# Kernel optimization log

Measured on AMD Instinct MI355X. Metric: run time of the kernel, lower is better.

Reference implementation:

```python
import jax, jax.numpy as jnp
import numpy as np

HEAD, D_MODEL, D_KV, D_FF = 12, 768, 64, 3072
BS, S = 8, 512
D_K = D_MODEL // HEAD


def layer_norm(x, g, b, eps=1e-5):
    m = jnp.mean(x, axis=-1, keepdims=True)
    v = jnp.var(x, axis=-1, keepdims=True)
    return (x - m) / jnp.sqrt(v + eps) * g + b


def setup_inputs() -> dict:
    key = jax.random.key(0)
    ks = jax.random.split(key, 16)
    w = lambda k, *s: (jax.random.normal(k, s, dtype=jnp.float32) * 0.02)
    return {
        'x': jax.random.normal(ks[0], (BS, S, D_MODEL), dtype=jnp.float32),
        'pad_mask': jnp.ones((BS, S), dtype=bool),
        'prior': jnp.zeros((1, 1, 1, 1), dtype=jnp.float32),
        # GroupAttention params
        'ga_ln_g': jnp.ones((D_MODEL,), jnp.float32), 'ga_ln_b': jnp.zeros((D_MODEL,), jnp.float32),
        'ga_wq': w(ks[1], D_K, D_K), 'ga_bq': jnp.zeros((D_K,), jnp.float32),
        'ga_wk': w(ks[2], D_K, D_K), 'ga_bk': jnp.zeros((D_K,), jnp.float32),
        # ScaledDotProductAttention params (head*d_kv == d_model)
        'sa_wq': w(ks[3], HEAD * D_KV, D_MODEL), 'sa_bq': jnp.zeros((HEAD * D_KV,), jnp.float32),
        'sa_wk': w(ks[4], HEAD * D_KV, D_MODEL), 'sa_bk': jnp.zeros((HEAD * D_KV,), jnp.float32),
        'sa_wv': w(ks[5], HEAD * D_KV, D_MODEL), 'sa_bv': jnp.zeros((HEAD * D_KV,), jnp.float32),
        # FFN params
        'ff_w1': w(ks[6], D_FF, D_MODEL), 'ff_b1': jnp.zeros((D_FF,), jnp.float32),
        'ff_w2': w(ks[7], D_MODEL, D_FF), 'ff_b2': jnp.zeros((D_MODEL,), jnp.float32),
        # Sublayer (pre-)norms
        'sl0_g': jnp.ones((D_MODEL,), jnp.float32), 'sl0_b': jnp.zeros((D_MODEL,), jnp.float32),
        'sl1_g': jnp.ones((D_MODEL,), jnp.float32), 'sl1_b': jnp.zeros((D_MODEL,), jnp.float32),
    }


def group_attention(x, pad_mask, prior, ln_g, ln_b, wq, bq, wk, bk):
    bs, s = x.shape[:2]
    ctx = layer_norm(x, ln_g, ln_b).reshape(bs, s, HEAD, D_K).transpose(0, 2, 1, 3)  # [bs,h,s,dk]
    a = jnp.eye(s, k=1, dtype=jnp.float32)   # superdiag
    c = jnp.eye(s, k=-1, dtype=jnp.float32)  # subdiag
    diag = jnp.eye(s, dtype=bool)
    tridiag = (a + c) > 0
    mask = pad_mask[:, None, None, :] & tridiag[None, None]  # [bs,1,s,s]
    q = ctx @ wq.T + bq
    k = ctx @ wk.T + bk
    scores = jnp.einsum('bhqd,bhkd->bhqk', q, k) / D_K
    scores = jnp.where(mask, scores, -10000.0)
    na = jax.nn.softmax(scores, axis=-1)
    na = jnp.sqrt(na * na.swapaxes(-2, -1) + 1e-4)
    na = prior + (1.0 - prior) * na
    tri = jnp.triu(jnp.ones((s, s), jnp.float32))  # upper incl diag
    # keep log-values only on the superdiagonal, zero elsewhere
    t = jnp.where(a[None, None] > 0, jnp.log(na + 1e-9), 0.0) @ tri
    g = jnp.exp(tri @ t)
    # zero where tri - eye == 0 (diagonal and strict lower) -> keep strict upper
    g = jnp.where((tri - jnp.eye(s, dtype=jnp.float32))[None, None] == 0, 0.0, g)
    g_attn = g + g.swapaxes(-2, -1) + jnp.where(diag[None, None], na, 1e-4)
    return g_attn, na


def self_attention(xn, group_prob, wq, bq, wk, bk, wv, bv):
    bs, s = xn.shape[:2]
    q = (xn @ wq.T + bq).reshape(bs, s, HEAD, D_KV).transpose(0, 2, 1, 3)
    k = (xn @ wk.T + bk).reshape(bs, s, HEAD, D_KV).transpose(0, 2, 1, 3)
    v = (xn @ wv.T + bv).reshape(bs, s, HEAD, D_KV).transpose(0, 2, 1, 3)
    att = jnp.einsum('bhqd,bhkd->bhqk', q, k) / np.sqrt(D_KV).astype(np.float32)
    # NOTE: original uses non-inplace att.masked_fill(...) without assignment -> mask has no effect
    att = jax.nn.softmax(att, axis=-1) * group_prob
    out = jnp.einsum('bhqk,bhkd->bhqd', att, v)
    return out.transpose(0, 2, 1, 3).reshape(bs, s, HEAD * D_KV)


def reference(x, pad_mask, prior,
              ga_ln_g, ga_ln_b, ga_wq, ga_bq, ga_wk, ga_bk,
              sa_wq, sa_bq, sa_wk, sa_bk, sa_wv, sa_bv,
              ff_w1, ff_b1, ff_w2, ff_b2,
              sl0_g, sl0_b, sl1_g, sl1_b):
    group_prob, break_prob = group_attention(x, pad_mask, prior,
                                             ga_ln_g, ga_ln_b, ga_wq, ga_bq, ga_wk, ga_bk)
    # sublayer 0: pre-norm residual around self-attn weighted by group_prob
    x = x + self_attention(layer_norm(x, sl0_g, sl0_b), group_prob,
                           sa_wq, sa_bq, sa_wk, sa_bk, sa_wv, sa_bv)
    # sublayer 1: pre-norm residual around FFN
    h = jax.nn.relu(layer_norm(x, sl1_g, sl1_b) @ ff_w1.T + ff_b1)
    x = x + (h @ ff_w2.T + ff_b2)
    return (x, group_prob, break_prob)
```

## Files before the change

### kernel.cpp

```cpp
#include <hip/hip_runtime.h>
#include <hip/hip_bf16.h>

#define HEADS 12
#define DM    768
#define DKH   64
#define DFF   3072
#define BSZ   8
#define SEQ   512
#define MROWS (BSZ*SEQ)
#define BH    (BSZ*HEADS)

typedef __attribute__((ext_vector_type(8))) short bf16x8;
typedef __attribute__((ext_vector_type(4))) float f32x4;

__device__ __forceinline__ void gload_lds16(const ushort* g, ushort* l) {
  __builtin_amdgcn_global_load_lds(
      (const __attribute__((address_space(1))) unsigned int*)g,
      (__attribute__((address_space(3))) unsigned int*)l, 16, 0, 0);
}

__device__ __forceinline__ float b2f(ushort u) {
  union { unsigned int i; float f; } c; c.i = (unsigned int)u << 16; return c.f;
}

__global__ __launch_bounds__(256) void ln_cvt_kernel(
    const float* __restrict__ x,
    const float* __restrict__ g0, const float* __restrict__ b0, __hip_bfloat16* __restrict__ ln0,
    const float* __restrict__ gg, const float* __restrict__ gb, __hip_bfloat16* __restrict__ lnga,
    const float* __restrict__ swq, const float* __restrict__ swk, const float* __restrict__ swv,
    const float* __restrict__ w1s, const float* __restrict__ w2s,
    __hip_bfloat16* __restrict__ dqkv, __hip_bfloat16* __restrict__ d1,
    __hip_bfloat16* __restrict__ d2) {
  int t = threadIdx.x;
  if (blockIdx.x >= 1024) {
    long gid = (long)(blockIdx.x - 1024)*256 + t;
    long i = gid*4;
    const float* s; __hip_bfloat16* d; long off;
    if (i < 1769472L) {
      long j = i / 589824L; off = i - j*589824L;
      s = (j == 0) ? swq : (j == 1) ? swk : swv;
      d = dqkv + j*589824L;
    } else if (i < 4128768L) {
      off = i - 1769472L; s = w1s; d = d1;
    } else {
      off = i - 4128768L; s = w2s; d = d2;
    }
    float4 v = *(const float4*)(s + off);
    d[off+0] = __float2bfloat16(v.x);
    d[off+1] = __float2bfloat16(v.y);
    d[off+2] = __float2bfloat16(v.z);
    d[off+3] = __float2bfloat16(v.w);
    return;
  }
  int lane = t & 63, w = t >> 6;
  int row = blockIdx.x*4 + w;
  size_t base = (size_t)row * DM;
  float v[12]; float s = 0.f, s2 = 0.f;
  #pragma unroll
  for (int i = 0; i < 12; ++i) {
    v[i] = x[base + lane + 64*i];
    s += v[i]; s2 += v[i]*v[i];
  }
  #pragma unroll
  for (int off = 1; off < 64; off <<= 1) {
    s  += __shfl_xor(s,  off, 64);
    s2 += __shfl_xor(s2, off, 64);
  }
  float mean = s * (1.f/DM);
  float rstd = rsqrtf(s2 * (1.f/DM) - mean*mean + 1e-5f);
  #pragma unroll
  for (int i = 0; i < 12; ++i) {
    int c = lane + 64*i;
    float h = (v[i]-mean)*rstd;
    ln0[base + c]  = __float2bfloat16(h*g0[c] + b0[c]);
    lnga[base + c] = __float2bfloat16(h*gg[c] + gb[c]);
  }
}

__global__ __launch_bounds__(256) void ga_proj_mfma_kernel(
    const __hip_bfloat16* __restrict__ lnga,
    const float* __restrict__ wq, const float* __restrict__ bq,
    const float* __restrict__ wk, const float* __restrict__ bk,
    float* __restrict__ Qg, float* __restrict__ Kg) {
  __shared__ ushort WQ[64*72];
  __shared__ ushort WK[64*72];
  int t = threadIdx.x;
  int h  = blockIdx.x >> 4;
  int r0 = (blockIdx.x & 15) * 256;
  for (int i = t; i < 4096; i += 256) {
    int d = i >> 6, c = i & 63;
    __hip_bfloat16 q = __float2bfloat16(wq[i]);
    __hip_bfloat16 k = __float2bfloat16(wk[i]);
    WQ[d*72 + c] = *(ushort*)&q;
    WK[d*72 + c] = *(ushort*)&k;
  }
  __syncthreads();
  int lane = t & 63, w = t >> 6;
  int lrow = lane & 15, lhi = lane >> 4;
  const ushort* Ag = (const ushort*)lnga;
  bf16x8 a[4][2];
  #pragma unroll
  for (int i = 0; i < 4; ++i)
    #pragma unroll
    for (int ks = 0; ks < 2; ++ks)
      a[i][ks] = *(const bf16x8*)(Ag + (size_t)(r0 + w*64 + i*16 + lrow)*DM + h*64 + ks*32 + lhi*8);
  int b = r0 >> 9;
  {
    bf16x8 bf[4][2];
    #pragma unroll
    for (int j = 0; j < 4; ++j)
      #pragma unroll
      for (int ks = 0; ks < 2; ++ks)
        bf[j][ks] = *(const bf16x8*)&WQ[(j*16 + lrow)*72 + ks*32 + lhi*8];
    f32x4 acc[4][4] = {};
    #pragma unroll
    for (int i = 0; i < 4; ++i)
      #pragma unroll
      for (int j = 0; j < 4; ++j) {
        acc[i][j] = __builtin_amdgcn_mfma_f32_16x16x32_bf16(a[i][0], bf[j][0], acc[i][j], 0, 0, 0);
        acc[i][j] = __builtin_amdgcn_mfma_f32_16x16x32_bf16(a[i][1], bf[j][1], acc[i][j], 0, 0, 0);
      }
    #pragma unroll
    for (int i = 0; i < 4; ++i) {
      int rowb = r0 + w*64 + i*16 + lhi*4;
      #pragma unroll
      for (int j = 0; j < 4; ++j) {
        int d = j*16 + lrow;
        float bias = bq[d];
        #pragma unroll
        for (int r = 0; r < 4; ++r) {
          int sIdx = (rowb + r) & 511;
          Qg[(((size_t)b*HEADS + h)*SEQ + sIdx)*DKH + d] = acc[i][j][r] + bias;
        }
      }
    }
  }
  {
    bf16x8 bf[4][2];
    #pragma unroll
    for (int j = 0; j < 4; ++j)
      #pragma unroll
      for (int ks = 0; ks < 2; ++ks)
        bf[j][ks] = *(const bf16x8*)&WK[(j*16 + lrow)*72 + ks*32 + lhi*8];
    f32x4 acc[4][4] = {};
    #pragma unroll
    for (int i = 0; i < 4; ++i)
      #pragma unroll
      for (int j = 0; j < 4; ++j) {
        acc[i][j] = __builtin_amdgcn_mfma_f32_16x16x32_bf16(a[i][0], bf[j][0], acc[i][j], 0, 0, 0);
        acc[i][j] = __builtin_amdgcn_mfma_f32_16x16x32_bf16(a[i][1], bf[j][1], acc[i][j], 0, 0, 0);
      }
    #pragma unroll
    for (int i = 0; i < 4; ++i) {
      int rowb = r0 + w*64 + i*16 + lhi*4;
      #pragma unroll
      for (int j = 0; j < 4; ++j) {
        int d = j*16 + lrow;
        float bias = bk[d];
        #pragma unroll
        for (int r = 0; r < 4; ++r) {
          int sIdx = (rowb + r) & 511;
          Kg[(((size_t)b*HEADS + h)*SEQ + sIdx)*DKH + d] = acc[i][j][r] + bias;
        }
      }
    }
  }
}

__global__ __launch_bounds__(512) void ga_edges_kernel(
    const float* __restrict__ Qg, const float* __restrict__ Kg,
    const float* __restrict__ prior, float* __restrict__ nsWS, float* __restrict__ cumWS) {
  __shared__ float pu[SEQ], pd[SEQ];
  __shared__ float wsum[8], wpre[8];
  int bh = blockIdx.x, m = threadIdx.x;
  const float* Qb = Qg + (size_t)bh*SEQ*DKH;
  const float* Kb = Kg + (size_t)bh*SEQ*DKH;
  const float4* qm = (const float4*)(Qb + (size_t)m*DKH);
  float su = -1e4f, sd = -1e4f;
  if (m < SEQ-1) {
    const float4* kn = (const float4*)(Kb + (size_t)(m+1)*DKH);
    float a = 0.f;
    #pragma unroll
    for (int i = 0; i < 16; ++i) {
      float4 q4 = qm[i], k4 = kn[i];
      a += q4.x*k4.x + q4.y*k4.y + q4.z*k4.z + q4.w*k4.w;
    }
    su = a * (1.f/DKH);
  }
  if (m >= 1) {
    const float4* kp = (const float4*)(Kb + (size_t)(m-1)*DKH);
    float a = 0.f;
    #pragma unroll
    for (int i = 0; i < 16; ++i) {
      float4 q4 = qm[i], k4 = kp[i];
      a += q4.x*k4.x + q4.y*k4.y + q4.z*k4.z + q4.w*k4.w;
    }
    sd = a * (1.f/DKH);
  }
  float mx = fmaxf(su, sd);
  float eu = __expf(su - mx), ed = __expf(sd - mx);
  float inv = 1.f / (eu + ed);
  pu[m] = eu * inv;
  pd[m] = ed * inv;
  __syncthreads();
  float pr = prior[0];
  float nsv = 0.f, lg = 0.f;
  if (m < SEQ-1) {
    float vv = sqrtf(pu[m]*pd[m+1] + 1e-4f);
    nsv = pr + (1.f - pr)*vv;
    lg = __logf(nsv + 1e-9f);
  }
  float v = lg;
  #pragma unroll
  for (int off = 1; off < 64; off <<= 1) {
    float u = __shfl_up(v, off, 64);
    if ((m & 63) >= off) v += u;
  }
  if ((m & 63) == 63) wsum[m >> 6] = v;
  __syncthreads();
  if (m == 0) {
    float a = 0.f;
    #pragma unroll
    for (int i = 0; i < 8; ++i) { wpre[i] = a; a += wsum[i]; }
  }
  __syncthreads();
  float incl = v + wpre[m >> 6];
  nsWS[(size_t)bh*SEQ + m] = nsv;
  cumWS[(size_t)bh*SEQ + m] = incl - lg;
}

template<int MODE>
__global__ __launch_bounds__(512, 2) void gemm256_kernel(
    const __hip_bfloat16* __restrict__ A, const __hip_bfloat16* __restrict__ B,
    const float* __restrict__ b0, const float* __restrict__ b1, const float* __restrict__ b2,
    __hip_bfloat16* __restrict__ C,
    const float* __restrict__ nsWS, const float* __restrict__ cumWS,
    const float* __restrict__ prior, float* __restrict__ gp, float* __restrict__ bp,
    int gbBase) {
  constexpr int N    = (MODE==0) ? 2304 : (MODE==1) ? 3072 : 768;
  constexpr int TN   = N / 256;
  constexpr int LDAB = (MODE==2) ? 3072 : 768;
  constexpr int NT   = (MODE==0) ? 144 : (MODE==1) ? 192 : 48;
  __shared__ ushort LDS[65536];
  int t = threadIdx.x;
  int bidx = blockIdx.x;
  if (MODE != 2 && bidx >= NT) {
    int gbBlk = gbBase + (bidx - NT);
    int bh = gbBlk >> 7;
    int q  = ((gbBlk & 127) << 2) | (t >> 7);
    int tt = t & 127;
    const float* cum = cumWS + (size_t)bh*SEQ;
    const float* ns  = nsWS  + (size_t)bh*SEQ;
    float pr = prior[0];
    float c0 = pr + (1.f - pr)*0.01f;
    float cq = cum[q];
    size_t rb = ((size_t)bh*SEQ + q)*SEQ;
    int k0 = tt*4;
    float4 g4, b4;
    float* gv = (float*)&g4; float* bv = (float*)&b4;
    #pragma unroll
    for (int j = 0; j < 4; ++j) {
      int k = k0 + j;
      float g;
      if (k == q) g = c0;
      else {
        float c = cum[k];
        g = __expf((k > q) ? (c - cq) : (cq - c)) + 1e-4f;
      }
      float bb = c0;
      if (k == q+1)      bb = ns[q];
      else if (k+1 == q) bb = ns[q-1];
      gv[j] = g; bv[j] = bb;
    }
    *(float4*)(gp + rb + k0) = g4;
    *(float4*)(bp + rb + k0) = b4;
    return;
  }
  int lane = t & 63, w = t >> 6;
  int rin = lane >> 3, gr = lane & 7;
  int lrow = lane & 15, lhi = lane >> 4;
  int tile = (bidx & 7)*(NT/8) + (bidx >> 3);
  int m0 = (tile / TN) * 256;
  int n0 = (tile % TN) * 256;
  int kOff = (MODE == 2) ? blockIdx.y * 768 : 0;
  if (MODE == 2) C += (size_t)blockIdx.y * MROWS * 768;
  int wr = w >> 2, wc = w & 3;
  const ushort* Ag = (const ushort*)A;
  const ushort* Bg = (const ushort*)B;
  f32x4 acc[8][4] = {};
  auto STAGE = [&](int p, int kt) {
    int k0 = kOff + kt*64;
    ushort* Ad = &LDS[p*16384];
    ushort* Bd = &LDS[32768 + p*16384];
    int cs = (gr ^ rin) * 8;
    #pragma unroll
    for (int q = 0; q < 4; ++q) {
      int rr = q*64 + w*8 + rin;
      gload_lds16(Ag + (size_t)(m0 + rr)*LDAB + k0 + cs, &Ad[(q*64 + w*8)*64]);
      gload_lds16(Bg + (size_t)(n0 + rr)*LDAB + k0 + cs, &Bd[(q*64 + w*8)*64]);
    }
  };
  const int nt = 12;
  STAGE(0, 0);
  STAGE(1, 1);
  asm volatile("s_waitcnt vmcnt(8)" ::: "memory");
  __builtin_amdgcn_s_barrier();
  int p = 0;
  for (int kt = 0; kt < nt; ++kt) {
    const ushort* Ar = &LDS[p*16384];
    const ushort* Br = &LDS[32768 + p*16384];
    int sw0 = (lhi ^ (lrow & 7)) * 8;
    int sw1 = ((4 + lhi) ^ (lrow & 7)) * 8;
    bf16x8 a0[8], b0r[4], a1[8], b1r[4];
    #pragma unroll
    for (int i = 0; i < 8; ++i)
      a0[i] = *(const bf16x8*)&Ar[(wr*128 + i*16 + lrow)*64 + sw0];
    #pragma unroll
    for (int j = 0; j < 4; ++j)
      b0r[j] = *(const bf16x8*)&Br[(wc*64 + j*16 + lrow)*64 + sw0];
    #pragma unroll
    for (int i = 0; i < 8; ++i)
      #pragma unroll
      for (int j = 0; j < 4; ++j)
        acc[i][j] = __builtin_amdgcn_mfma_f32_16x16x32_bf16(a0[i], b0r[j], acc[i][j], 0, 0, 0);
    #pragma unroll
    for (int i = 0; i < 8; ++i)
      a1[i] = *(const bf16x8*)&Ar[(wr*128 + i*16 + lrow)*64 + sw1];
    #pragma unroll
    for (int j = 0; j < 4; ++j)
      b1r[j] = *(const bf16x8*)&Br[(wc*64 + j*16 + lrow)*64 + sw1];
    asm volatile("s_waitcnt lgkmcnt(0)" ::: "memory");
    __builtin_amdgcn_sched_barrier(0);
    __builtin_amdgcn_s_barrier();
    if (kt + 2 < nt) STAGE(p, kt + 2);
    __builtin_amdgcn_s_setprio(1);
    #pragma unroll
    for (int i = 0; i < 8; ++i)
      #pragma unroll
      for (int j = 0; j < 4; ++j)
        acc[i][j] = __builtin_amdgcn_mfma_f32_16x16x32_bf16(a1[i], b1r[j], acc[i][j], 0, 0, 0);
    __builtin_amdgcn_s_setprio(0);
    if (kt + 1 < nt) {
      if (kt + 2 < nt) asm volatile("s_waitcnt vmcnt(8)" ::: "memory");
      else             asm volatile("s_waitcnt vmcnt(0)" ::: "memory");
      __builtin_amdgcn_s_barrier();
    }
    p ^= 1;
  }
  #pragma unroll
  for (int i = 0; i < 8; ++i) {
    int grow = m0 + wr*128 + i*16 + lhi*4;
    #pragma unroll
    for (int j = 0; j < 4; ++j) {
      int gcol = n0 + wc*64 + j*16 + lrow;
      float bvv;
      if (MODE == 0)      bvv = (gcol < 768) ? b0[gcol] : (gcol < 1536) ? b1[gcol-768] : b2[gcol-1536];
      else if (MODE == 1) bvv = b0[gcol];
      else                bvv = 0.f;
      #pragma unroll
      for (int r = 0; r < 4; ++r) {
        float v = acc[i][j][r] + bvv;
        if (MODE == 1) v = fmaxf(v, 0.f);
        C[(size_t)(grow + r)*N + gcol] = __float2bfloat16(v);
      }
    }
  }
}

__global__ __launch_bounds__(256) void vt_kernel(
    const __hip_bfloat16* __restrict__ qkv, __hip_bfloat16* __restrict__ vT) {
  int gid = blockIdx.x*256 + threadIdx.x;
  int o = gid*8;
  int bh = o >> 15;
  int rem = o & 32767;
  int d = rem >> 9;
  int s0 = rem & 511;
  int b = bh / HEADS, h = bh % HEADS;
  const ushort* src = (const ushort*)qkv + ((size_t)(b*SEQ + s0))*2304 + 1536 + h*64 + d;
  ushort tmp[8];
  #pragma unroll
  for (int j = 0; j < 8; ++j) tmp[j] = src[(size_t)j*2304];
  *(bf16x8*)((ushort*)vT + (size_t)bh*32768 + d*512 + s0) = *(bf16x8*)tmp;
}

__global__ __launch_bounds__(256) void ffn2_reduce_kernel(
    const __hip_bfloat16* __restrict__ p, const float* __restrict__ bias,
    float* __restrict__ out) {
  int gid = blockIdx.x*256 + threadIdx.x;
  size_t i = (size_t)gid*8;
  const ushort* pp = (const ushort*)p;
  float acc[8];
  int col = (int)(i % DM);
  #pragma unroll
  for (int j = 0; j < 8; ++j) acc[j] = bias[col + j];
  #pragma unroll
  for (int s = 0; s < 4; ++s) {
    bf16x8 v = *(const bf16x8*)(pp + (size_t)s*MROWS*DM + i);
    #pragma unroll
    for (int j = 0; j < 8; ++j) acc[j] += b2f((ushort)v[j]);
  }
  float4 o0 = *(const float4*)(out + i);
  float4 o1 = *(const float4*)(out + i + 4);
  o0.x += acc[0]; o0.y += acc[1]; o0.z += acc[2]; o0.w += acc[3];
  o1.x += acc[4]; o1.y += acc[5]; o1.z += acc[6]; o1.w += acc[7];
  *(float4*)(out + i)     = o0;
  *(float4*)(out + i + 4) = o1;
}

__global__ __launch_bounds__(256) void ln_res_kernel(
    const float* __restrict__ x, const __hip_bfloat16* __restrict__ a, float* __restrict__ xs,
    const float* __restrict__ g, const float* __restrict__ b, __hip_bfloat16* __restrict__ o) {
  __shared__ float lds[16];
  int row = blockIdx.x, t = threadIdx.x;
  size_t base = (size_t)row * DM;
  float v0 = x[base+t]     + __bfloat162float(a[base+t]);
  float v1 = x[base+t+256] + __bfloat162float(a[base+t+256]);
  float v2 = x[base+t+512] + __bfloat162float(a[base+t+512]);
  xs[base+t] = v0; xs[base+t+256] = v1; xs[base+t+512] = v2;
  float s = v0 + v1 + v2, s2 = v0*v0 + v1*v1 + v2*v2;
  #pragma unroll
  for (int off = 32; off > 0; off >>= 1) {
    s  += __shfl_down(s,  off, 64);
    s2 += __shfl_down(s2, off, 64);
  }
  int w = t >> 6, ln = t & 63;
  if (ln == 0) { lds[w*2] = s; lds[w*2+1] = s2; }
  __syncthreads();
  if (t == 0) {
    float aa = 0.f, bb = 0.f;
    for (int i = 0; i < 4; ++i) { aa += lds[i*2]; bb += lds[i*2+1]; }
    lds[0] = aa; lds[1] = bb;
  }
  __syncthreads();
  s = lds[0]; s2 = lds[1];
  float mean = s * (1.f/DM);
  float rstd = rsqrtf(s2 * (1.f/DM) - mean*mean + 1e-5f);
  o[base+t]     = __float2bfloat16((v0-mean)*rstd*g[t]     + b[t]);
  o[base+t+256] = __float2bfloat16((v1-mean)*rstd*g[t+256] + b[t+256]);
  o[base+t+512] = __float2bfloat16((v2-mean)*rstd*g[t+512] + b[t+512]);
}

__global__ __launch_bounds__(256) void attn_mfma_kernel(
    const __hip_bfloat16* __restrict__ qk, const __hip_bfloat16* __restrict__ vT,
    const float* __restrict__ cumWS, const float* __restrict__ prior,
    __hip_bfloat16* __restrict__ att) {
  __shared__ ushort Ps[4][16][72];
  int t = threadIdx.x;
  int lane = t & 63, wid = t >> 6;
  int bid = blockIdx.x + blockIdx.y * 8;
  int tile = (bid & 7)*96 + (bid >> 3);
  int qt = tile & 7, bh = tile >> 3;
  int b = bh / HEADS, h = bh % HEADS;
  int lrow = lane & 15, lhi = lane >> 4;
  int qbase = qt*64 + wid*16;
  const ushort* qg = (const ushort*)qk;
  bf16x8 aq[2];
  {
    const ushort* qp = qg + (size_t)(b*SEQ + qbase + lrow)*2304 + h*64 + lhi*8;
    aq[0] = *(const bf16x8*)qp;
    aq[1] = *(const bf16x8*)(qp + 32);
  }
  const float* cum = cumWS + (size_t)bh*SEQ;
  float pr = prior[0];
  float c0 = pr + (1.f - pr)*0.01f;
  int qrow[4]; float cq[4];
  #pragma unroll
  for (int r = 0; r < 4; ++r) { qrow[r] = qbase + lhi*4 + r; cq[r] = cum[qrow[r]]; }
  float lsum[4] = {0.f, 0.f, 0.f, 0.f};
  f32x4 oacc[4] = {};
  const ushort* kg = qg + 768;
  const ushort* vg = (const ushort*)vT;
  for (int kt = 0; kt < 8; ++kt) {
    f32x4 sacc[4] = {};
    #pragma unroll
    for (int j = 0; j < 4; ++j) {
      const ushort* kp = kg + (size_t)(b*SEQ + kt*64 + j*16 + lrow)*2304 + h*64 + lhi*8;
      bf16x8 bk0 = *(const bf16x8*)kp;
      bf16x8 bk1 = *(const bf16x8*)(kp + 32);
      sacc[j] = __builtin_amdgcn_mfma_f32_16x16x32_bf16(aq[0], bk0, sacc[j], 0, 0, 0);
      sacc[j] = __builtin_amdgcn_mfma_f32_16x16x32_bf16(aq[1], bk1, sacc[j], 0, 0, 0);
    }
    float ck[4];
    #pragma unroll
    for (int j = 0; j < 4; ++j) ck[j] = cum[kt*64 + j*16 + lrow];
    #pragma unroll
    for (int j = 0; j < 4; ++j) {
      int kk = kt*64 + j*16 + lrow;
      #pragma unroll
      for (int r = 0; r < 4; ++r) {
        float e = __expf(fminf(sacc[j][r]*0.125f - 16.f, 60.f));
        lsum[r] += e;
        float dd = ck[j] - cq[r];
        float gpv = (kk == qrow[r]) ? c0 : (__expf((kk > qrow[r]) ? dd : -dd) + 1e-4f);
        __hip_bfloat16 pb = __float2bfloat16(e * gpv);
        Ps[wid][lhi*4 + r][j*16 + lrow] = *(ushort*)&pb;
      }
    }
    asm volatile("s_waitcnt lgkmcnt(0)" ::: "memory");
    #pragma unroll
    for (int c = 0; c < 2; ++c) {
      bf16x8 ap = *(const bf16x8*)&Ps[wid][lrow][c*32 + lhi*8];
      #pragma unroll
      for (int dj = 0; dj < 4; ++dj) {
        const ushort* vp = vg + ((size_t)bh*64 + dj*16 + lrow)*512 + kt*64 + c*32 + lhi*8;
        bf16x8 bv = *(const bf16x8*)vp;
        oacc[dj] = __builtin_amdgcn_mfma_f32_16x16x32_bf16(ap, bv, oacc[dj], 0, 0, 0);
      }
    }
  }
  #pragma unroll
  for (int off = 1; off < 16; off <<= 1) {
    #pragma unroll
    for (int r = 0; r < 4; ++r) lsum[r] += __shfl_xor(lsum[r], off, 64);
  }
  float inv[4];
  #pragma unroll
  for (int r = 0; r < 4; ++r) inv[r] = 1.f / lsum[r];
  #pragma unroll
  for (int dj = 0; dj < 4; ++dj) {
    #pragma unroll
    for (int r = 0; r < 4; ++r) {
      float v = oacc[dj][r] * inv[r];
      att[(size_t)(b*SEQ + qbase + lhi*4 + r)*DM + h*64 + dj*16 + lrow] = __float2bfloat16(v);
    }
  }
}

extern "C" void kernel_launch(void* const* d_in, const int* in_sizes, int n_in,
                              void* d_out, int out_size, void* d_ws, size_t ws_size,
                              hipStream_t stream) {
  const float* x      = (const float*)d_in[0];
  const float* prior  = (const float*)d_in[2];
  const float* ga_g   = (const float*)d_in[3];
  const float* ga_b   = (const float*)d_in[4];
  const float* ga_wq  = (const float*)d_in[5];
  const float* ga_bq  = (const float*)d_in[6];
  const float* ga_wk  = (const float*)d_in[7];
  const float* ga_bk  = (const float*)d_in[8];
  const float* sa_wq  = (const float*)d_in[9];
  const float* sa_bq  = (const float*)d_in[10];
  const float* sa_wk  = (const float*)d_in[11];
  const float* sa_bk  = (const float*)d_in[12];
  const float* sa_wv  = (const float*)d_in[13];
  const float* sa_bv  = (const float*)d_in[14];
  const float* ff_w1  = (const float*)d_in[15];
  const float* ff_b1  = (const float*)d_in[16];
  const float* ff_w2  = (const float*)d_in[17];
  const float* ff_b2  = (const float*)d_in[18];
  const float* sl0_g  = (const float*)d_in[19];
  const float* sl0_b  = (const float*)d_in[20];
  const float* sl1_g  = (const float*)d_in[21];
  const float* sl1_b  = (const float*)d_in[22];

  float* out_x  = (float*)d_out;
  float* out_gp = out_x  + (size_t)MROWS*DM;
  float* out_bp = out_gp + (size_t)BH*SEQ*SEQ;

  char* W = (char*)d_ws;
  __hip_bfloat16* ln0    = (__hip_bfloat16*)(W + 0);
  __hip_bfloat16* lnga   = (__hip_bfloat16*)(W + 6291456);
  float* Qg   = (float*)(W + 12582912);
  float* Kg   = (float*)(W + 25165824);
  __hip_bfloat16* qkv3   = (__hip_bfloat16*)(W + 37748736);
  __hip_bfloat16* vT     = (__hip_bfloat16*)(W + 56623104);
  __hip_bfloat16* attbuf = (__hip_bfloat16*)(W + 62914560);
  __hip_bfloat16* ln1    = (__hip_bfloat16*)(W + 69206016);
  __hip_bfloat16* wqkv   = (__hip_bfloat16*)(W + 75497472);
  __hip_bfloat16* w1     = (__hip_bfloat16*)(W + 79036416);
  __hip_bfloat16* w2     = (__hip_bfloat16*)(W + 83755008);
  __hip_bfloat16* hbuf   = (__hip_bfloat16*)(W + 88473600);
  __hip_bfloat16* parts  = (__hip_bfloat16*)(W + 113639424);
  float* nsWS  = (float*)(W + 138805248);
  float* cumWS = (float*)(W + 139001856);

  ln_cvt_kernel<<<7360, 256, 0, stream>>>(
      x, sl0_g, sl0_b, ln0, ga_g, ga_b, lnga,
      sa_wq, sa_wk, sa_wv, ff_w1, ff_w2, wqkv, w1, w2);
  ga_proj_mfma_kernel<<<192, 256, 0, stream>>>(lnga, ga_wq, ga_bq, ga_wk, ga_bk, Qg, Kg);
  ga_edges_kernel<<<BH, SEQ, 0, stream>>>(Qg, Kg, prior, nsWS, cumWS);
  gemm256_kernel<0><<<144 + 6144, 512, 0, stream>>>(
      ln0, wqkv, sa_bq, sa_bk, sa_bv, qkv3,
      nsWS, cumWS, prior, out_gp, out_bp, 0);
  vt_kernel<<<3072, 256, 0, stream>>>(qkv3, vT);
  attn_mfma_kernel<<<dim3(8, BH), 256, 0, stream>>>(qkv3, vT, cumWS, prior, attbuf);
  ln_res_kernel<<<MROWS, 256, 0, stream>>>(x, attbuf, out_x, sl1_g, sl1_b, ln1);
  gemm256_kernel<1><<<192 + 6144, 512, 0, stream>>>(
      ln1, w1, ff_b1, nullptr, nullptr, hbuf,
      nsWS, cumWS, prior, out_gp, out_bp, 6144);
  gemm256_kernel<2><<<dim3(48, 4), 512, 0, stream>>>(
      hbuf, w2, nullptr, nullptr, nullptr, parts,
      nullptr, nullptr, nullptr, nullptr, nullptr, 0);
  ffn2_reduce_kernel<<<1536, 256, 0, stream>>>(parts, ff_b2, out_x);
}
```

Measured before the change: 279.1 us.

## Fuse GA projection into QKV GEMM, transpose V in epilogue, spread gp/bp writes

```diff
diff --git a/kernel.cpp b/kernel.cpp
--- a/kernel.cpp
+++ b/kernel.cpp
@@ -21,6 +21,69 @@
 
 __device__ __forceinline__ float b2f(ushort u) {
   union { unsigned int i; float f; } c; c.i = (unsigned int)u << 16; return c.f;
+}
+
+__device__ __forceinline__ void gb_rows_512(
+    int row, int t, const float* __restrict__ nsWS, const float* __restrict__ cumWS,
+    const float* __restrict__ prior, float* __restrict__ gp, float* __restrict__ bp) {
+  int bh = row >> 9, q = row & 511;
+  const float* cum = cumWS + (size_t)bh*SEQ;
+  const float* ns  = nsWS  + (size_t)bh*SEQ;
+  float pr = prior[0];
+  float c0 = pr + (1.f - pr)*0.01f;
+  float cq = cum[q];
+  size_t rb = ((size_t)bh*SEQ + q)*SEQ;
+  int k0 = (t & 127)*4;
+  float4 g4, b4;
+  float* gv = (float*)&g4; float* bv = (float*)&b4;
+  #pragma unroll
+  for (int j = 0; j < 4; ++j) {
+    int k = k0 + j;
+    float g;
+    if (k == q) g = c0;
+    else {
+      float c = cum[k];
+      g = __expf((k > q) ? (c - cq) : (cq - c)) + 1e-4f;
+    }
+    float bb = c0;
+    if (k == q+1)      bb = ns[q];
+    else if (k+1 == q) bb = ns[q-1];
+    gv[j] = g; bv[j] = bb;
+  }
+  *(float4*)(gp + rb + k0) = g4;
+  *(float4*)(bp + rb + k0) = b4;
+}
+
+__device__ __forceinline__ void gb_rows_256(
+    int row, int t, const float* __restrict__ nsWS, const float* __restrict__ cumWS,
+    const float* __restrict__ prior, float* __restrict__ gp, float* __restrict__ bp) {
+  int bh = row >> 9, q = row & 511;
+  const float* cum = cumWS + (size_t)bh*SEQ;
+  const float* ns  = nsWS  + (size_t)bh*SEQ;
+  float pr = prior[0];
+  float c0 = pr + (1.f - pr)*0.01f;
+  float cq = cum[q];
+  size_t rb = ((size_t)bh*SEQ + q)*SEQ;
+  int k0 = (t & 63)*8;
+  float g8[8], b8[8];
+  #pragma unroll
+  for (int j = 0; j < 8; ++j) {
+    int k = k0 + j;
+    float g;
+    if (k == q) g = c0;
+    else {
+      float c = cum[k];
+      g = __expf((k > q) ? (c - cq) : (cq - c)) + 1e-4f;
+    }
+    float bb = c0;
+    if (k == q+1)      bb = ns[q];
+    else if (k+1 == q) bb = ns[q-1];
+    g8[j] = g; b8[j] = bb;
+  }
+  *(float4*)(gp + rb + k0)     = *(float4*)&g8[0];
+  *(float4*)(gp + rb + k0 + 4) = *(float4*)&g8[4];
+  *(float4*)(bp + rb + k0)     = *(float4*)&b8[0];
+  *(float4*)(bp + rb + k0 + 4) = *(float4*)&b8[4];
 }
 
 __global__ __launch_bounds__(256) void ln_cvt_kernel(
@@ -77,96 +140,6 @@
   }
 }
 
-__global__ __launch_bounds__(256) void ga_proj_mfma_kernel(
-    const __hip_bfloat16* __restrict__ lnga,
-    const float* __restrict__ wq, const float* __restrict__ bq,
-    const float* __restrict__ wk, const float* __restrict__ bk,
-    float* __restrict__ Qg, float* __restrict__ Kg) {
-  __shared__ ushort WQ[64*72];
-  __shared__ ushort WK[64*72];
-  int t = threadIdx.x;
-  int h  = blockIdx.x >> 4;
-  int r0 = (blockIdx.x & 15) * 256;
-  for (int i = t; i < 4096; i += 256) {
-    int d = i >> 6, c = i & 63;
-    __hip_bfloat16 q = __float2bfloat16(wq[i]);
-    __hip_bfloat16 k = __float2bfloat16(wk[i]);
-    WQ[d*72 + c] = *(ushort*)&q;
-    WK[d*72 + c] = *(ushort*)&k;
-  }
-  __syncthreads();
-  int lane = t & 63, w = t >> 6;
-  int lrow = lane & 15, lhi = lane >> 4;
-  const ushort* Ag = (const ushort*)lnga;
-  bf16x8 a[4][2];
-  #pragma unroll
-  for (int i = 0; i < 4; ++i)
-    #pragma unroll
-    for (int ks = 0; ks < 2; ++ks)
-      a[i][ks] = *(const bf16x8*)(Ag + (size_t)(r0 + w*64 + i*16 + lrow)*DM + h*64 + ks*32 + lhi*8);
-  int b = r0 >> 9;
-  {
-    bf16x8 bf[4][2];
-    #pragma unroll
-    for (int j = 0; j < 4; ++j)
-      #pragma unroll
-      for (int ks = 0; ks < 2; ++ks)
-        bf[j][ks] = *(const bf16x8*)&WQ[(j*16 + lrow)*72 + ks*32 + lhi*8];
-    f32x4 acc[4][4] = {};
-    #pragma unroll
-    for (int i = 0; i < 4; ++i)
-      #pragma unroll
-      for (int j = 0; j < 4; ++j) {
-        acc[i][j] = __builtin_amdgcn_mfma_f32_16x16x32_bf16(a[i][0], bf[j][0], acc[i][j], 0, 0, 0);
-        acc[i][j] = __builtin_amdgcn_mfma_f32_16x16x32_bf16(a[i][1], bf[j][1], acc[i][j], 0, 0, 0);
-      }
-    #pragma unroll
-    for (int i = 0; i < 4; ++i) {
-      int rowb = r0 + w*64 + i*16 + lhi*4;
-      #pragma unroll
-      for (int j = 0; j < 4; ++j) {
-        int d = j*16 + lrow;
-        float bias = bq[d];
-        #pragma unroll
-        for (int r = 0; r < 4; ++r) {
-          int sIdx = (rowb + r) & 511;
-          Qg[(((size_t)b*HEADS + h)*SEQ + sIdx)*DKH + d] = acc[i][j][r] + bias;
-        }
-      }
-    }
-  }
-  {
-    bf16x8 bf[4][2];
-    #pragma unroll
-    for (int j = 0; j < 4; ++j)
-      #pragma unroll
-      for (int ks = 0; ks < 2; ++ks)
-        bf[j][ks] = *(const bf16x8*)&WK[(j*16 + lrow)*72 + ks*32 + lhi*8];
-    f32x4 acc[4][4] = {};
-    #pragma unroll
-    for (int i = 0; i < 4; ++i)
-      #pragma unroll
-      for (int j = 0; j < 4; ++j) {
-        acc[i][j] = __builtin_amdgcn_mfma_f32_16x16x32_bf16(a[i][0], bf[j][0], acc[i][j], 0, 0, 0);
-        acc[i][j] = __builtin_amdgcn_mfma_f32_16x16x32_bf16(a[i][1], bf[j][1], acc[i][j], 0, 0, 0);
-      }
-    #pragma unroll
-    for (int i = 0; i < 4; ++i) {
-      int rowb = r0 + w*64 + i*16 + lhi*4;
-      #pragma unroll
-      for (int j = 0; j < 4; ++j) {
-        int d = j*16 + lrow;
-        float bias = bk[d];
-        #pragma unroll
-        for (int r = 0; r < 4; ++r) {
-          int sIdx = (rowb + r) & 511;
-          Kg[(((size_t)b*HEADS + h)*SEQ + sIdx)*DKH + d] = acc[i][j][r] + bias;
-        }
-      }
-    }
-  }
-}
-
 __global__ __launch_bounds__(512) void ga_edges_kernel(
     const float* __restrict__ Qg, const float* __restrict__ Kg,
     const float* __restrict__ prior, float* __restrict__ nsWS, float* __restrict__ cumWS) {
@@ -233,57 +206,98 @@
 __global__ __launch_bounds__(512, 2) void gemm256_kernel(
     const __hip_bfloat16* __restrict__ A, const __hip_bfloat16* __restrict__ B,
     const float* __restrict__ b0, const float* __restrict__ b1, const float* __restrict__ b2,
-    __hip_bfloat16* __restrict__ C,
+    __hip_bfloat16* __restrict__ C, __hip_bfloat16* __restrict__ vT,
     const float* __restrict__ nsWS, const float* __restrict__ cumWS,
     const float* __restrict__ prior, float* __restrict__ gp, float* __restrict__ bp,
-    int gbBase) {
+    const __hip_bfloat16* __restrict__ lnga,
+    const float* __restrict__ gwq, const float* __restrict__ gbq,
+    const float* __restrict__ gwk, const float* __restrict__ gbk,
+    float* __restrict__ Qg, float* __restrict__ Kg) {
   constexpr int N    = (MODE==0) ? 2304 : (MODE==1) ? 3072 : 768;
   constexpr int TN   = N / 256;
   constexpr int LDAB = (MODE==2) ? 3072 : 768;
-  constexpr int NT   = (MODE==0) ? 144 : (MODE==1) ? 192 : 48;
+  constexpr int NT   = (MODE==0) ? 144 : (MODE==1) ? 192 : 192;
   __shared__ ushort LDS[65536];
   int t = threadIdx.x;
   int bidx = blockIdx.x;
-  if (MODE != 2 && bidx >= NT) {
-    int gbBlk = gbBase + (bidx - NT);
-    int bh = gbBlk >> 7;
-    int q  = ((gbBlk & 127) << 2) | (t >> 7);
-    int tt = t & 127;
-    const float* cum = cumWS + (size_t)bh*SEQ;
-    const float* ns  = nsWS  + (size_t)bh*SEQ;
-    float pr = prior[0];
-    float c0 = pr + (1.f - pr)*0.01f;
-    float cq = cum[q];
-    size_t rb = ((size_t)bh*SEQ + q)*SEQ;
-    int k0 = tt*4;
-    float4 g4, b4;
-    float* gv = (float*)&g4; float* bv = (float*)&b4;
-    #pragma unroll
-    for (int j = 0; j < 4; ++j) {
-      int k = k0 + j;
-      float g;
-      if (k == q) g = c0;
-      else {
-        float c = cum[k];
-        g = __expf((k > q) ? (c - cq) : (cq - c)) + 1e-4f;
+  if (bidx >= NT) {
+    if (MODE == 0) {
+      ushort* WQ = LDS;
+      ushort* WK = LDS + 4608;
+      for (int i = t; i < 4096; i += 512) {
+        int d = i >> 6, c = i & 63;
+        __hip_bfloat16 q = __float2bfloat16(gwq[i]);
+        __hip_bfloat16 k = __float2bfloat16(gwk[i]);
+        WQ[d*72 + c] = *(ushort*)&q;
+        WK[d*72 + c] = *(ushort*)&k;
       }
-      float bb = c0;
-      if (k == q+1)      bb = ns[q];
-      else if (k+1 == q) bb = ns[q-1];
-      gv[j] = g; bv[j] = bb;
-    }
-    *(float4*)(gp + rb + k0) = g4;
-    *(float4*)(bp + rb + k0) = b4;
+      __syncthreads();
+      int task = (bidx - 144)*2 + (t >> 8);
+      int h  = task >> 4;
+      int r0 = (task & 15) * 256;
+      int t2 = t & 255;
+      int lane = t2 & 63, w = t2 >> 6;
+      int lrow = lane & 15, lhi = lane >> 4;
+      const ushort* Ag2 = (const ushort*)lnga;
+      bf16x8 a[4][2];
+      #pragma unroll
+      for (int i = 0; i < 4; ++i)
+        #pragma unroll
+        for (int ks = 0; ks < 2; ++ks)
+          a[i][ks] = *(const bf16x8*)(Ag2 + (size_t)(r0 + w*64 + i*16 + lrow)*DM + h*64 + ks*32 + lhi*8);
+      int b = r0 >> 9;
+      #pragma unroll
+      for (int qk = 0; qk < 2; ++qk) {
+        const ushort* Wm = qk ? WK : WQ;
+        const float* bias = qk ? gbk : gbq;
+        float* Og = qk ? Kg : Qg;
+        bf16x8 bf[4][2];
+        #pragma unroll
+        for (int j = 0; j < 4; ++j)
+          #pragma unroll
+          for (int ks = 0; ks < 2; ++ks)
+            bf[j][ks] = *(const bf16x8*)&Wm[(j*16 + lrow)*72 + ks*32 + lhi*8];
+        f32x4 acc[4][4] = {};
+        #pragma unroll
+        for (int i = 0; i < 4; ++i)
+          #pragma unroll
+          for (int j = 0; j < 4; ++j) {
+            acc[i][j] = __builtin_amdgcn_mfma_f32_16x16x32_bf16(a[i][0], bf[j][0], acc[i][j], 0, 0, 0);
+            acc[i][j] = __builtin_amdgcn_mfma_f32_16x16x32_bf16(a[i][1], bf[j][1], acc[i][j], 0, 0, 0);
+          }
+        #pragma unroll
+        for (int i = 0; i < 4; ++i) {
+          int rowb = r0 + w*64 + i*16 + lhi*4;
+          #pragma unroll
+          for (int j = 0; j < 4; ++j) {
+            int d = j*16 + lrow;
+            float bv = bias[d];
+            #pragma unroll
+            for (int r = 0; r < 4; ++r) {
+              int sIdx = (rowb + r) & 511;
+              Og[(((size_t)b*HEADS + h)*SEQ + sIdx)*DKH + d] = acc[i][j][r] + bv;
+            }
+          }
+        }
+      }
+    } else {
+      int base = (MODE == 1) ? 16384 : 32768;
+      int row = base + (bidx - NT)*4 + (t >> 7);
+      gb_rows_512(row, t, nsWS, cumWS, prior, gp, bp);
+    }
     return;
   }
   int lane = t & 63, w = t >> 6;
   int rin = lane >> 3, gr = lane & 7;
   int lrow = lane & 15, lhi = lane >> 4;
-  int tile = (bidx & 7)*(NT/8) + (bidx >> 3);
+  int z = 0, tl = bidx;
+  if (MODE == 2) { z = bidx / 48; tl = bidx % 48; }
+  constexpr int NTIL = (MODE==2) ? 48 : NT;
+  int tile = (tl & 7)*(NTIL/8) + (tl >> 3);
   int m0 = (tile / TN) * 256;
   int n0 = (tile % TN) * 256;
-  int kOff = (MODE == 2) ? blockIdx.y * 768 : 0;
-  if (MODE == 2) C += (size_t)blockIdx.y * MROWS * 768;
+  int kOff = (MODE == 2) ? z * 768 : 0;
+  if (MODE == 2) C += (size_t)z * MROWS * 768;
   int wr = w >> 2, wc = w & 3;
   const ushort* Ag = (const ushort*)A;
   const ushort* Bg = (const ushort*)B;
@@ -347,6 +361,40 @@
     }
     p ^= 1;
   }
+  if (MODE == 0 && n0 >= 1536) {
+    ushort* T = LDS;
+    int b = m0 >> 9, s0 = m0 & 511;
+    #pragma unroll
+    for (int ps = 0; ps < 2; ++ps) {
+      if ((wc >> 1) == ps) {
+        #pragma unroll
+        for (int j = 0; j < 4; ++j) {
+          int dl = (wc & 1)*64 + j*16 + lrow;
+          float bvv = b2[n0 - 1536 + ps*128 + dl];
+          #pragma unroll
+          for (int i = 0; i < 8; ++i) {
+            #pragma unroll
+            for (int r = 0; r < 4; ++r) {
+              __hip_bfloat16 hh = __float2bfloat16(acc[i][j][r] + bvv);
+              T[dl*264 + wr*128 + i*16 + lhi*4 + r] = *(ushort*)&hh;
+            }
+          }
+        }
+      }
+      __syncthreads();
+      #pragma unroll
+      for (int it = 0; it < 8; ++it) {
+        int idx = t + 512*it;
+        int dl = idx >> 5, sc8 = (idx & 31)*8;
+        int dg = n0 - 1536 + ps*128 + dl;
+        int h = dg >> 6, dmod = dg & 63;
+        bf16x8 vv = *(const bf16x8*)&T[dl*264 + sc8];
+        *(bf16x8*)((ushort*)vT + ((size_t)(b*HEADS + h)*64 + dmod)*512 + s0 + sc8) = vv;
+      }
+      __syncthreads();
+    }
+    return;
+  }
   #pragma unroll
   for (int i = 0; i < 8; ++i) {
     int grow = m0 + wr*128 + i*16 + lhi*4;
@@ -354,7 +402,7 @@
     for (int j = 0; j < 4; ++j) {
       int gcol = n0 + wc*64 + j*16 + lrow;
       float bvv;
-      if (MODE == 0)      bvv = (gcol < 768) ? b0[gcol] : (gcol < 1536) ? b1[gcol-768] : b2[gcol-1536];
+      if (MODE == 0)      bvv = (gcol < 768) ? b0[gcol] : b1[gcol-768];
       else if (MODE == 1) bvv = b0[gcol];
       else                bvv = 0.f;
       #pragma unroll
@@ -365,22 +413,6 @@
       }
     }
   }
-}
-
-__global__ __launch_bounds__(256) void vt_kernel(
-    const __hip_bfloat16* __restrict__ qkv, __hip_bfloat16* __restrict__ vT) {
-  int gid = blockIdx.x*256 + threadIdx.x;
-  int o = gid*8;
-  int bh = o >> 15;
-  int rem = o & 32767;
-  int d = rem >> 9;
-  int s0 = rem & 511;
-  int b = bh / HEADS, h = bh % HEADS;
-  const ushort* src = (const ushort*)qkv + ((size_t)(b*SEQ + s0))*2304 + 1536 + h*64 + d;
-  ushort tmp[8];
-  #pragma unroll
-  for (int j = 0; j < 8; ++j) tmp[j] = src[(size_t)j*2304];
-  *(bf16x8*)((ushort*)vT + (size_t)bh*32768 + d*512 + s0) = *(bf16x8*)tmp;
 }
 
 __global__ __launch_bounds__(256) void ffn2_reduce_kernel(
@@ -410,45 +442,48 @@
 __global__ __launch_bounds__(256) void ln_res_kernel(
     const float* __restrict__ x, const __hip_bfloat16* __restrict__ a, float* __restrict__ xs,
     const float* __restrict__ g, const float* __restrict__ b, __hip_bfloat16* __restrict__ o) {
-  __shared__ float lds[16];
-  int row = blockIdx.x, t = threadIdx.x;
+  int t = threadIdx.x;
+  int lane = t & 63, w = t >> 6;
+  int row = blockIdx.x*4 + w;
   size_t base = (size_t)row * DM;
-  float v0 = x[base+t]     + __bfloat162float(a[base+t]);
-  float v1 = x[base+t+256] + __bfloat162float(a[base+t+256]);
-  float v2 = x[base+t+512] + __bfloat162float(a[base+t+512]);
-  xs[base+t] = v0; xs[base+t+256] = v1; xs[base+t+512] = v2;
-  float s = v0 + v1 + v2, s2 = v0*v0 + v1*v1 + v2*v2;
-  #pragma unroll
-  for (int off = 32; off > 0; off >>= 1) {
-    s  += __shfl_down(s,  off, 64);
-    s2 += __shfl_down(s2, off, 64);
-  }
-  int w = t >> 6, ln = t & 63;
-  if (ln == 0) { lds[w*2] = s; lds[w*2+1] = s2; }
-  __syncthreads();
-  if (t == 0) {
-    float aa = 0.f, bb = 0.f;
-    for (int i = 0; i < 4; ++i) { aa += lds[i*2]; bb += lds[i*2+1]; }
-    lds[0] = aa; lds[1] = bb;
-  }
-  __syncthreads();
-  s = lds[0]; s2 = lds[1];
+  const ushort* ab = (const ushort*)a;
+  float v[12]; float s = 0.f, s2 = 0.f;
+  #pragma unroll
+  for (int i = 0; i < 12; ++i) {
+    int c = lane + 64*i;
+    v[i] = x[base + c] + b2f(ab[base + c]);
+    xs[base + c] = v[i];
+    s += v[i]; s2 += v[i]*v[i];
+  }
+  #pragma unroll
+  for (int off = 1; off < 64; off <<= 1) {
+    s  += __shfl_xor(s,  off, 64);
+    s2 += __shfl_xor(s2, off, 64);
+  }
   float mean = s * (1.f/DM);
   float rstd = rsqrtf(s2 * (1.f/DM) - mean*mean + 1e-5f);
-  o[base+t]     = __float2bfloat16((v0-mean)*rstd*g[t]     + b[t]);
-  o[base+t+256] = __float2bfloat16((v1-mean)*rstd*g[t+256] + b[t+256]);
-  o[base+t+512] = __float2bfloat16((v2-mean)*rstd*g[t+512] + b[t+512]);
+  #pragma unroll
+  for (int i = 0; i < 12; ++i) {
+    int c = lane + 64*i;
+    o[base + c] = __float2bfloat16((v[i]-mean)*rstd*g[c] + b[c]);
+  }
 }
 
 __global__ __launch_bounds__(256) void attn_mfma_kernel(
     const __hip_bfloat16* __restrict__ qk, const __hip_bfloat16* __restrict__ vT,
     const float* __restrict__ cumWS, const float* __restrict__ prior,
-    __hip_bfloat16* __restrict__ att) {
+    __hip_bfloat16* __restrict__ att,
+    const float* __restrict__ nsWS, float* __restrict__ gp, float* __restrict__ bp) {
   __shared__ ushort Ps[4][16][72];
   int t = threadIdx.x;
+  int bidx = blockIdx.x;
+  if (bidx >= 768) {
+    int row = (bidx - 768)*4 + (t >> 6);
+    gb_rows_256(row, t, nsWS, cumWS, prior, gp, bp);
+    return;
+  }
   int lane = t & 63, wid = t >> 6;
-  int bid = blockIdx.x + blockIdx.y * 8;
-  int tile = (bid & 7)*96 + (bid >> 3);
+  int tile = (bidx & 7)*96 + (bidx >> 3);
   int qt = tile & 7, bh = tile >> 3;
   int b = bh / HEADS, h = bh % HEADS;
   int lrow = lane & 15, lhi = lane >> 4;
@@ -576,19 +611,21 @@
   ln_cvt_kernel<<<7360, 256, 0, stream>>>(
       x, sl0_g, sl0_b, ln0, ga_g, ga_b, lnga,
       sa_wq, sa_wk, sa_wv, ff_w1, ff_w2, wqkv, w1, w2);
-  ga_proj_mfma_kernel<<<192, 256, 0, stream>>>(lnga, ga_wq, ga_bq, ga_wk, ga_bk, Qg, Kg);
+  gemm256_kernel<0><<<240, 512, 0, stream>>>(
+      ln0, wqkv, sa_bq, sa_bk, sa_bv, qkv3, vT,
+      nullptr, nullptr, nullptr, nullptr, nullptr,
+      lnga, ga_wq, ga_bq, ga_wk, ga_bk, Qg, Kg);
   ga_edges_kernel<<<BH, SEQ, 0, stream>>>(Qg, Kg, prior, nsWS, cumWS);
-  gemm256_kernel<0><<<144 + 6144, 512, 0, stream>>>(
-      ln0, wqkv, sa_bq, sa_bk, sa_bv, qkv3,
-      nsWS, cumWS, prior, out_gp, out_bp, 0);
-  vt_kernel<<<3072, 256, 0, stream>>>(qkv3, vT);
-  attn_mfma_kernel<<<dim3(8, BH), 256, 0, stream>>>(qkv3, vT, cumWS, prior, attbuf);
-  ln_res_kernel<<<MROWS, 256, 0, stream>>>(x, attbuf, out_x, sl1_g, sl1_b, ln1);
-  gemm256_kernel<1><<<192 + 6144, 512, 0, stream>>>(
-      ln1, w1, ff_b1, nullptr, nullptr, hbuf,
-      nsWS, cumWS, prior, out_gp, out_bp, 6144);
-  gemm256_kernel<2><<<dim3(48, 4), 512, 0, stream>>>(
-      hbuf, w2, nullptr, nullptr, nullptr, parts,
-      nullptr, nullptr, nullptr, nullptr, nullptr, 0);
+  attn_mfma_kernel<<<768 + 4096, 256, 0, stream>>>(
+      qkv3, vT, cumWS, prior, attbuf, nsWS, out_gp, out_bp);
+  ln_res_kernel<<<1024, 256, 0, stream>>>(x, attbuf, out_x, sl1_g, sl1_b, ln1);
+  gemm256_kernel<1><<<192 + 4096, 512, 0, stream>>>(
+      ln1, w1, ff_b1, nullptr, nullptr, hbuf, nullptr,
+      nsWS, cumWS, prior, out_gp, out_bp,
+      nullptr, nullptr, nullptr, nullptr, nullptr, nullptr, nullptr);
+  gemm256_kernel<2><<<192 + 4096, 512, 0, stream>>>(
+      hbuf, w2, nullptr, nullptr, nullptr, parts, nullptr,
+      nsWS, cumWS, prior, out_gp, out_bp,
+      nullptr, nullptr, nullptr, nullptr, nullptr, nullptr, nullptr);
   ffn2_reduce_kernel<<<1536, 256, 0, stream>>>(parts, ff_b2, out_x);
 }
```

New measurement: 235.9 us. 15.5% less time.
